# Optimization experiments

Hardware: AMD Instinct MI355X
Metric: run time of the kernel (lower is better)

## Reference

```python
import jax, jax.numpy as jnp
import numpy as np

B, Q, K, D, H = 2, 2048, 2048, 1024, 16
HD = D // H  # 64
EPS = 1e-6  # flax LayerNorm default epsilon


def setup_inputs() -> dict:
    key = jax.random.key(0)
    ks = jax.random.split(key, 12)
    s = 1.0 / np.sqrt(D)  # lecun_normal-like scale
    inputs_q = jax.random.normal(ks[0], (B, Q, D), jnp.float32)
    bias = jax.random.normal(ks[1], (B, 1, Q, K), jnp.float32)
    mask = jax.random.randint(ks[2], (B, 1, Q, K), 0, 2).astype(jnp.bool_)
    wq = jax.random.normal(ks[3], (D, H, HD), jnp.float32) * s
    wk = jax.random.normal(ks[4], (D, H, HD), jnp.float32) * s
    wv = jax.random.normal(ks[5], (D, H, HD), jnp.float32) * s
    bq = jnp.zeros((H, HD), jnp.float32)
    bk = jnp.zeros((H, HD), jnp.float32)
    bv = jnp.zeros((H, HD), jnp.float32)
    q_scale = jnp.ones((HD,), jnp.float32)
    k_scale = jnp.ones((HD,), jnp.float32)
    wo = jax.random.normal(ks[6], (H, HD, D), jnp.float32) * s
    bo = jnp.zeros((D,), jnp.float32)
    return dict(inputs_q=inputs_q, bias=bias, mask=mask, wq=wq, bq=bq,
                wk=wk, bk=bk, wv=wv, bv=bv, q_scale=q_scale, k_scale=k_scale,
                wo=wo, bo=bo)


def _layernorm_nobias(x, scale):
    # normalize over last axis (head_dim), no bias, like flax LayerNorm(use_bias=False)
    mean = jnp.mean(x, axis=-1, keepdims=True)
    var = jnp.mean(jnp.square(x - mean), axis=-1, keepdims=True)
    return (x - mean) * jax.lax.rsqrt(var + EPS) * scale


def reference(inputs_q, bias, mask, wq, bq, wk, bk, wv, bv, q_scale, k_scale, wo, bo):
    # QKV projections (self-attention: k and v inputs default to inputs_q)
    q = jnp.einsum('bqd,dhe->bqhe', inputs_q, wq) + bq  # [B,Q,H,HD]
    k = jnp.einsum('bkd,dhe->bkhe', inputs_q, wk) + bk  # [B,K,H,HD]
    v = jnp.einsum('bkd,dhe->bkhe', inputs_q, wv) + bv  # [B,K,H,HD]
    # optional QK layernorm (normalize_qk=True)
    q = _layernorm_nobias(q, q_scale)
    k = _layernorm_nobias(k, k_scale)
    # attention weights
    q = q / jnp.sqrt(jnp.asarray(q.shape[-1], q.dtype))
    attn = jnp.einsum('bqhe,bkhe->bhqk', q, k)  # [B,H,Q,K]
    attn = attn + bias
    big_neg = jnp.finfo(q.dtype).min
    attn = jnp.where(mask, attn, big_neg)
    attn = jax.nn.softmax(attn.astype(jnp.float32), axis=-1).astype(q.dtype)
    # weighted values + output projection
    x = jnp.einsum('bhqk,bkhe->bqhe', attn, v)  # [B,Q,H,HD]
    out = jnp.einsum('bqhe,heo->bqo', x, wo) + bo  # [B,Q,D]
    return out
```

## Files before the change

kernel.cpp:

```cpp
#include <hip/hip_runtime.h>
#include <cstdint>
#include <cstddef>

typedef __bf16 bf16_t;
typedef __bf16 bf16x8 __attribute__((ext_vector_type(8)));
typedef __bf16 bf16x4 __attribute__((ext_vector_type(4)));
typedef _Float16 f16_t;
typedef _Float16 f16x4 __attribute__((ext_vector_type(4)));
typedef float f32x4 __attribute__((ext_vector_type(4)));

constexpr int BB = 2, SS = 2048, DD = 1024, HH = 16, HDIM = 64;
constexpr int BS = BB * SS;
constexpr float LOG2E = 1.4426950408889634f;

__device__ __forceinline__ void glds16(const void* g, void* l) {
  __builtin_amdgcn_global_load_lds((const __attribute__((address_space(1))) void*)g,
                                   (__attribute__((address_space(3))) void*)l, 16, 0, 0);
}

__global__ __launch_bounds__(256) void prep_fused(
    const float* __restrict__ x, const float* __restrict__ wq, const float* __restrict__ wk,
    const float* __restrict__ wv, const float* __restrict__ wo, const float* __restrict__ bias,
    const int* __restrict__ mask, bf16_t* __restrict__ xb, bf16_t* __restrict__ wqkv_t,
    bf16_t* __restrict__ wo_t, f16_t* __restrict__ vmq) {
  __shared__ __align__(16) char smem[18432];
  float (*tile)[65] = (float(*)[65])smem;
  f16_t (*btile)[72] = (f16_t(*)[72])smem;
  int bid = blockIdx.x;
  int t = threadIdx.x;
  if (bid < 4096) {
    int i = bid * 256 + t;
    float4 v = ((const float4*)x)[i];
    union { bf16_t h[4]; uint2 u; } o;
    o.h[0] = (bf16_t)v.x; o.h[1] = (bf16_t)v.y; o.h[2] = (bf16_t)v.z; o.h[3] = (bf16_t)v.w;
    ((uint2*)xb)[i] = o.u;
  } else if (bid < 5120) {
    int id = bid - 4096;
    int which = id >> 8, tr = (id >> 4) & 15, tc = id & 15;
    const float* src = (which == 0) ? wq : (which == 1) ? wk : (which == 2) ? wv : wo;
    bf16_t* dst = (which < 3) ? wqkv_t : wo_t;
    int noff = (which < 3) ? which * 1024 : 0;
#pragma unroll
    for (int p = 0; p < 4; ++p) {
      int e = (p * 256 + t) * 4;
      int r = e >> 6, c = e & 63;
      float4 v = *(const float4*)&src[(size_t)(tr * 64 + r) * 1024 + tc * 64 + c];
      tile[r][c] = v.x; tile[r][c + 1] = v.y; tile[r][c + 2] = v.z; tile[r][c + 3] = v.w;
    }
    __syncthreads();
#pragma unroll
    for (int p = 0; p < 4; ++p) {
      int e = (p * 256 + t) * 4;
      int r = e >> 6, c = e & 63;
      union { bf16_t h[4]; uint2 u; } o;
#pragma unroll
      for (int j = 0; j < 4; ++j) o.h[j] = (bf16_t)tile[c + j][r];
      *(uint2*)&dst[(size_t)(noff + tc * 64 + r) * 1024 + tr * 64 + c] = o.u;
    }
  } else {
    int id = bid - 5120;
    int b = id >> 9, qt = (id >> 5) & 15, kt = id & 31;
    size_t base_in = ((size_t)(b * 2048 + qt * 128)) * 2048 + kt * 64;
#pragma unroll
    for (int p = 0; p < 4; ++p) {
      int c = p * 256 + t;
      int qr = c >> 3, k8 = (c & 7) * 8;
      const float* bp = &bias[base_in + (size_t)qr * 2048 + k8];
      const int* mp = &mask[base_in + (size_t)qr * 2048 + k8];
      float4 b0 = *(const float4*)bp;
      float4 b1 = *(const float4*)(bp + 4);
      int4 m0 = *(const int4*)mp;
      int4 m1 = *(const int4*)(mp + 4);
      union { f16_t h[8]; uint4 u; } o;
      o.h[0] = m0.x ? (f16_t)__builtin_amdgcn_exp2f(b0.x * LOG2E - 8.0f) : (f16_t)0.0f;
      o.h[1] = m0.y ? (f16_t)__builtin_amdgcn_exp2f(b0.y * LOG2E - 8.0f) : (f16_t)0.0f;
      o.h[2] = m0.z ? (f16_t)__builtin_amdgcn_exp2f(b0.z * LOG2E - 8.0f) : (f16_t)0.0f;
      o.h[3] = m0.w ? (f16_t)__builtin_amdgcn_exp2f(b0.w * LOG2E - 8.0f) : (f16_t)0.0f;
      o.h[4] = m1.x ? (f16_t)__builtin_amdgcn_exp2f(b1.x * LOG2E - 8.0f) : (f16_t)0.0f;
      o.h[5] = m1.y ? (f16_t)__builtin_amdgcn_exp2f(b1.y * LOG2E - 8.0f) : (f16_t)0.0f;
      o.h[6] = m1.z ? (f16_t)__builtin_amdgcn_exp2f(b1.z * LOG2E - 8.0f) : (f16_t)0.0f;
      o.h[7] = m1.w ? (f16_t)__builtin_amdgcn_exp2f(b1.w * LOG2E - 8.0f) : (f16_t)0.0f;
      *(uint4*)&btile[qr][k8] = o.u;
    }
    __syncthreads();
    int w = t >> 6, lane = t & 63, lo = lane & 15, quad = lane >> 4;
    size_t obase = ((size_t)(((b * 16 + qt) * 32 + kt) * 16)) * 64;
#pragma unroll
    for (int j = 0; j < 4; ++j) {
      int row = w * 32 + (j >> 1) * 16 + lo;
      int mbl = 2 * (j & 1);
      union { f16_t h[8]; uint4 u; } o;
#pragma unroll
      for (int e = 0; e < 8; ++e)
        o.h[e] = btile[row][(mbl + (e >> 2)) * 16 + quad * 4 + (e & 3)];
      ((uint4*)vmq)[obase + (w * 4 + j) * 64 + lane] = o.u;
    }
  }
}

template <bool OUT_F32, int BNT>
__global__ __launch_bounds__(256) void gemm_bt(const bf16_t* __restrict__ A,
                                               const bf16_t* __restrict__ Bt,
                                               bf16_t* __restrict__ Cb, float* __restrict__ Cf,
                                               const float* __restrict__ bias, int M, int N,
                                               int Kd) {
  constexpr int WNW = BNT / 2;
  constexpr int NFR = WNW / 16;
  __shared__ __align__(16) bf16_t As[128][32];
  __shared__ __align__(16) bf16_t Bs[BNT][32];
  int tid = threadIdx.x;
  int lane = tid & 63, w = tid >> 6;
  int lo = lane & 15, quad = lane >> 4;
  int wm = w >> 1, wn = w & 1;
  int nbx = gridDim.x;
  int nwg = nbx * gridDim.y;
  int lid = blockIdx.y * nbx + blockIdx.x;
  int sid = (lid & 7) * (nwg >> 3) + (lid >> 3);
  int m0 = (sid / nbx) * 128, n0 = (sid % nbx) * BNT;
  int srow = lane >> 2;
  int scol = (lane & 3) * 8;
  f32x4 acc[4][NFR] = {};
  for (int kk = 0; kk < Kd; kk += 32) {
#pragma unroll
    for (int t = 0; t < 2; ++t) {
      int rb = (w * 2 + t) * 16;
      glds16(&A[(size_t)(m0 + rb + srow) * Kd + kk + scol], &As[rb][0]);
      if (rb < BNT) glds16(&Bt[(size_t)(n0 + rb + srow) * Kd + kk + scol], &Bs[rb][0]);
    }
    asm volatile("s_waitcnt vmcnt(0)" ::: "memory");
    __syncthreads();
    bf16x8 am[4], bn[NFR];
#pragma unroll
    for (int i = 0; i < 4; ++i) am[i] = *(const bf16x8*)&As[wm * 64 + i * 16 + lo][quad * 8];
#pragma unroll
    for (int i = 0; i < NFR; ++i) bn[i] = *(const bf16x8*)&Bs[wn * WNW + i * 16 + lo][quad * 8];
#pragma unroll
    for (int mi = 0; mi < 4; ++mi)
#pragma unroll
      for (int ni = 0; ni < NFR; ++ni)
        acc[mi][ni] = __builtin_amdgcn_mfma_f32_16x16x32_bf16(am[mi], bn[ni], acc[mi][ni], 0, 0, 0);
    __syncthreads();
  }
#pragma unroll
  for (int mi = 0; mi < 4; ++mi) {
#pragma unroll
    for (int ni = 0; ni < NFR; ++ni) {
#pragma unroll
      for (int r = 0; r < 4; ++r) {
        int row = m0 + wm * 64 + mi * 16 + quad * 4 + r;
        int col = n0 + wn * WNW + ni * 16 + lo;
        float v = acc[mi][ni][r];
        if (OUT_F32)
          Cf[(size_t)row * N + col] = v + bias[col];
        else
          Cb[(size_t)row * N + col] = (bf16_t)v;
      }
    }
  }
}

__global__ __launch_bounds__(256) void postqkv(const bf16_t* __restrict__ Cqkv,
                                               const float* __restrict__ bq,
                                               const float* __restrict__ bk,
                                               const float* __restrict__ bv,
                                               const float* __restrict__ q_scale,
                                               const float* __restrict__ k_scale,
                                               bf16_t* __restrict__ qb, bf16_t* __restrict__ kb,
                                               f16_t* __restrict__ vt) {
  __shared__ float tile[64][65];
  int bid = blockIdx.x;
  int t = threadIdx.x;
  if (bid < 4096) {
    int mode = bid >> 11;
    int lane = t & 63;
    const float* badd = (mode == 0) ? bq : bk;
    const float* sc = (mode == 0) ? q_scale : k_scale;
    bf16_t* dst = (mode == 0) ? qb : kb;
    int vb = (bid & 2047) * 32 + (t >> 6) * 8;
#pragma unroll
    for (int i = 0; i < 8; ++i) {
      int vec = vb + i;
      int bs = vec >> 4, h = vec & 15;
      int b = bs >> 11, s = bs & 2047;
      float x = (float)Cqkv[(size_t)bs * 3072 + mode * 1024 + h * 64 + lane] + badd[h * 64 + lane];
      float sum = x;
#pragma unroll
      for (int off = 32; off >= 1; off >>= 1) sum += __shfl_xor(sum, off, 64);
      float mean = sum * (1.0f / 64.0f);
      float d = x - mean;
      float vs = d * d;
#pragma unroll
      for (int off = 32; off >= 1; off >>= 1) vs += __shfl_xor(vs, off, 64);
      float var = vs * (1.0f / 64.0f);
      float y = d * rsqrtf(var + 1e-6f) * sc[lane];
      if (mode == 0) y *= 0.125f * LOG2E;
      int el = (mode == 0) ? lane : ((((lane >> 3) ^ (s & 7)) << 3) | (lane & 7));
      dst[(size_t)((b * 16 + h) * 2048 + s) * 64 + el] = (bf16_t)y;
    }
  } else {
    int id2 = bid - 4096;
    int st = id2 & 31, h = (id2 >> 5) & 15, b = id2 >> 9;
#pragma unroll
    for (int p = 0; p < 2; ++p) {
      int e = (p * 256 + t) * 8;
      int r = e >> 6, c = e & 63;
      bf16x8 v8 = *(const bf16x8*)&Cqkv[(size_t)(b * SS + st * 64 + r) * 3072 + 2048 + h * 64 + c];
#pragma unroll
      for (int j = 0; j < 8; ++j) tile[r][c + j] = (float)v8[j] + bv[h * 64 + c + j];
    }
    __syncthreads();
#pragma unroll
    for (int p = 0; p < 2; ++p) {
      int e = (p * 256 + t) * 8;
      int r = e >> 6, c = e & 63;
      union { f16_t h[8]; uint4 u; } o;
#pragma unroll
      for (int j = 0; j < 8; ++j) o.h[j] = (f16_t)tile[c + j][r];
      *(uint4*)&vt[(size_t)((b * HH + h) * HDIM + r) * SS + st * 64 +
                   ((((c >> 3) ^ (r & 7)) << 3))] = o.u;
    }
  }
}

#define ATTN_TILE(KT, CUR, STG, VMC)                                                          \
  {                                                                                           \
    if ((KT) == 31) { asm volatile("s_waitcnt vmcnt(0)" ::: "memory"); }                      \
    else            { asm volatile("s_waitcnt vmcnt(8)" ::: "memory"); }                      \
    __builtin_amdgcn_s_barrier();                                                             \
    if ((KT) + 2 < 32) {                                                                      \
      int k0n = ((KT) + 2) * 64;                                                              \
      _Pragma("unroll") for (int tt = 0; tt < 2; ++tt) {                                      \
        int i = w * 2 + tt;                                                                   \
        int r = i * 8 + (lane >> 3);                                                          \
        glds16(&kbase[(size_t)(k0n + r) * 64 + ((lane & 7) << 3)], (STG) + i * 1024);         \
        glds16(&vbase[(size_t)r * SS + k0n + ((lane & 7) << 3)], (STG) + 8192 + i * 1024);    \
      }                                                                                       \
    }                                                                                         \
    __builtin_amdgcn_s_setprio(1);                                                            \
    bf16x8 ka[4][2];                                                                          \
    _Pragma("unroll") for (int mb = 0; mb < 4; ++mb)                                          \
      _Pragma("unroll") for (int ec = 0; ec < 2; ++ec)                                        \
        ka[mb][ec] = *(const bf16x8*)((CUR) + (mb * 16 + lo) * 128 +                          \
                                      ((((ec << 2) | quad) ^ (lo & 7)) << 4));                \
    f16x4 pf[2][4];                                                                           \
    _Pragma("unroll") for (int qg = 0; qg < 2; ++qg)                                          \
      _Pragma("unroll") for (int mb = 0; mb < 4; ++mb) {                                      \
        f32x4 s = {};                                                                         \
        s = __builtin_amdgcn_mfma_f32_16x16x32_bf16(ka[mb][0], bqf[qg][0], s, 0, 0, 0);       \
        s = __builtin_amdgcn_mfma_f32_16x16x32_bf16(ka[mb][1], bqf[qg][1], s, 0, 0, 0);       \
        f16x4 p4;                                                                             \
        p4[0] = (f16_t)__builtin_amdgcn_exp2f(fminf(s[0], 15.0f));                            \
        p4[1] = (f16_t)__builtin_amdgcn_exp2f(fminf(s[1], 15.0f));                            \
        p4[2] = (f16_t)__builtin_amdgcn_exp2f(fminf(s[2], 15.0f));                            \
        p4[3] = (f16_t)__builtin_amdgcn_exp2f(fminf(s[3], 15.0f));                            \
        pf[qg][mb] = p4 * VMC[qg * 2 + (mb >> 1)].q[mb & 1];                                  \
      }                                                                                       \
    __builtin_amdgcn_s_setprio(0);                                                            \
    if ((KT) + 2 < 32) {           \
      _Pragma("unroll") for (int j = 0; j < 4; ++j)                                           \
        VMC[j].u = vmtile[(size_t)((KT) + 2) * 1024 + j * 64];                                \
    }                                                                                         \
    __builtin_amdgcn_s_setprio(1);                                                            \
    _Pragma("unroll") for (int mb = 0; mb < 4; ++mb) {                                        \
      _Pragma("unroll") for (int eb = 0; eb < 4; ++eb) {                                      \
        f16x4 va = *(const f16x4*)((CUR) + 8192 + (eb * 16 + lo) * 128 +                      \
                                   (((((mb << 1) | (quad >> 1)) ^ (lo & 7)) << 4) |           \
                                    ((quad & 1) << 3)));                                      \
        _Pragma("unroll") for (int qg = 0; qg < 2; ++qg)                                      \
          ot[qg][eb] =                                                                        \
              __builtin_amdgcn_mfma_f32_16x16x16f16(va, pf[qg][mb], ot[qg][eb], 0, 0, 0);     \
      }                                                                                       \
      _Pragma("unroll") for (int qg = 0; qg < 2; ++qg)                                        \
        lacc[qg] = __builtin_amdgcn_mfma_f32_16x16x16f16(ones, pf[qg][mb], lacc[qg], 0, 0, 0);\
    }                                                                                         \
    __builtin_amdgcn_s_setprio(0);                                                            \
  }

__global__ __launch_bounds__(256, 2) void attn_kernel(const bf16_t* __restrict__ qb,
                                                      const bf16_t* __restrict__ kb,
                                                      const f16_t* __restrict__ vt,
                                                      const f16_t* __restrict__ vmq,
                                                      bf16_t* __restrict__ xout) {
  __shared__ __align__(16) char lds[4][16384];
  int tid = threadIdx.x;
  int lane = tid & 63, w = tid >> 6;
  int lo = lane & 15, quad = lane >> 4;
  int qt = blockIdx.x, h = blockIdx.y, b = blockIdx.z;
  size_t headoff = (size_t)(b * HH + h) * SS * HDIM;
  int q0 = qt * 128 + w * 32;
  const bf16_t* kbase = kb + headoff;
  const f16_t* vbase = vt + headoff;
  const uint4* vmtile =
      (const uint4*)vmq + ((size_t)((b * 16 + qt) * 32) * 16 + w * 4) * 64 + lane;

  bf16x8 bqf[2][2];
#pragma unroll
  for (int qg = 0; qg < 2; ++qg)
#pragma unroll
    for (int ec = 0; ec < 2; ++ec)
      bqf[qg][ec] =
          *(const bf16x8*)&qb[headoff + (size_t)(q0 + qg * 16 + lo) * HDIM + ec * 32 + quad * 8];

  f16x4 ones;
#pragma unroll
  for (int j = 0; j < 4; ++j) ones[j] = (f16_t)1.0f;

  f32x4 ot[2][4] = {};
  f32x4 lacc[2] = {};

  union VM { uint4 u; f16x4 q[2]; };
  VM vma[4], vmb[4];

#pragma unroll
  for (int tt = 0; tt < 2; ++tt) {
    int i = w * 2 + tt;
    int r = i * 8 + (lane >> 3);
    glds16(&kbase[(size_t)r * 64 + ((lane & 7) << 3)], lds[0] + i * 1024);
    glds16(&vbase[(size_t)r * SS + ((lane & 7) << 3)], lds[0] + 8192 + i * 1024);
  }
#pragma unroll
  for (int j = 0; j < 4; ++j) vma[j].u = vmtile[j * 64];
#pragma unroll
  for (int tt = 0; tt < 2; ++tt) {
    int i = w * 2 + tt;
    int r = i * 8 + (lane >> 3);
    glds16(&kbase[(size_t)(64 + r) * 64 + ((lane & 7) << 3)], lds[1] + i * 1024);
    glds16(&vbase[(size_t)r * SS + 64 + ((lane & 7) << 3)], lds[1] + 8192 + i * 1024);
  }
#pragma unroll
  for (int j = 0; j < 4; ++j) vmb[j].u = vmtile[1024 + j * 64];

#pragma unroll 1
  for (int kt0 = 0; kt0 < 32; kt0 += 4) {
    ATTN_TILE(kt0 + 0, lds[0], lds[2], vma)
    ATTN_TILE(kt0 + 1, lds[1], lds[3], vmb)
    ATTN_TILE(kt0 + 2, lds[2], lds[0], vma)
    ATTN_TILE(kt0 + 3, lds[3], lds[1], vmb)
  }

#pragma unroll
  for (int qg = 0; qg < 2; ++qg) {
    float rl = 1.0f / lacc[qg][0];
    int q = q0 + qg * 16 + lo;
#pragma unroll
    for (int eb = 0; eb < 4; ++eb) {
      union { bf16_t h4[4]; uint2 u; } o;
#pragma unroll
      for (int r = 0; r < 4; ++r) o.h4[r] = (bf16_t)(ot[qg][eb][r] * rl);
      *(uint2*)&xout[(size_t)(b * SS + q) * DD + h * 64 + eb * 16 + quad * 4] = o.u;
    }
  }
}

extern "C" void kernel_launch(void* const* d_in, const int* in_sizes, int n_in, void* d_out,
                              int out_size, void* d_ws, size_t ws_size, hipStream_t stream) {
  const float* inputs_q = (const float*)d_in[0];
  const float* bias = (const float*)d_in[1];
  const int* mask = (const int*)d_in[2];
  const float* wq = (const float*)d_in[3];
  const float* bq = (const float*)d_in[4];
  const float* wk = (const float*)d_in[5];
  const float* bk = (const float*)d_in[6];
  const float* wv = (const float*)d_in[7];
  const float* bv = (const float*)d_in[8];
  const float* q_scale = (const float*)d_in[9];
  const float* k_scale = (const float*)d_in[10];
  const float* wo = (const float*)d_in[11];
  const float* bo = (const float*)d_in[12];
  float* out = (float*)d_out;

  char* ws = (char*)d_ws;
  bf16_t* wo_t   = (bf16_t*)(ws);
  f16_t*  vmq    = (f16_t*)(ws + ((size_t)2 << 20));
  bf16_t* cqkv   = (bf16_t*)(ws + ((size_t)19 << 20));
  bf16_t* xattn  = (bf16_t*)(ws + ((size_t)19 << 20));
  bf16_t* xb     = (bf16_t*)(ws + ((size_t)43 << 20));
  bf16_t* qb2    = (bf16_t*)(ws + ((size_t)43 << 20));
  bf16_t* wqkv_t = (bf16_t*)(ws + ((size_t)51 << 20));
  bf16_t* kb2    = (bf16_t*)(ws + ((size_t)51 << 20));
  f16_t*  vtb    = (f16_t*)(ws + ((size_t)59 << 20));

  prep_fused<<<6144, 256, 0, stream>>>(inputs_q, wq, wk, wv, wo, bias, mask, xb, wqkv_t, wo_t, vmq);
  gemm_bt<false, 128><<<dim3(24, 32), 256, 0, stream>>>(xb, wqkv_t, cqkv, nullptr, nullptr, BS,
                                                        3072, DD);
  postqkv<<<5120, 256, 0, stream>>>(cqkv, bq, bk, bv, q_scale, k_scale, qb2, kb2, vtb);
  attn_kernel<<<dim3(SS / 128, HH, BB), 256, 0, stream>>>(qb2, kb2, vtb, vmq, xattn);
  gemm_bt<true, 64><<<dim3(16, 32), 256, 0, stream>>>(xattn, wo_t, nullptr, out, bo, BS, 1024, DD);
}
```

Before: 285.8 us.

## Split attention over two key halves with a merge kernel

The attention grid is split along the key dimension into two halves, doubling the block count. Each block writes unnormalized fp16 partial outputs and row sums to workspace, and a new merge kernel adds the halves and normalizes into bf16. LDS triple-buffering replaces the four buffers with rotating pointers so three blocks can fit per CU. The cost is extra global traffic for the partials, one more launch, and fp16 range risk on unnormalized accumulators (exponents are clamped, so the max-free softmax still applies).

```diff
diff --git a/kernel.cpp b/kernel.cpp
--- a/kernel.cpp
+++ b/kernel.cpp
@@ -224,10 +224,10 @@
 
 #define ATTN_TILE(KT, CUR, STG, VMC)                                                          \
   {                                                                                           \
-    if ((KT) == 31) { asm volatile("s_waitcnt vmcnt(0)" ::: "memory"); }                      \
+    if ((KT) == 15) { asm volatile("s_waitcnt vmcnt(0)" ::: "memory"); }                      \
     else            { asm volatile("s_waitcnt vmcnt(8)" ::: "memory"); }                      \
     __builtin_amdgcn_s_barrier();                                                             \
-    if ((KT) + 2 < 32) {                                                                      \
+    if ((KT) + 2 < 16) {                                                                      \
       int k0n = ((KT) + 2) * 64;                                                              \
       _Pragma("unroll") for (int tt = 0; tt < 2; ++tt) {                                      \
         int i = w * 2 + tt;                                                                   \
@@ -256,7 +256,7 @@
         pf[qg][mb] = p4 * VMC[qg * 2 + (mb >> 1)].q[mb & 1];                                  \
       }                                                                                       \
     __builtin_amdgcn_s_setprio(0);                                                            \
-    if ((KT) + 2 < 32) {           \
+    if ((KT) + 2 < 16) {           \
       _Pragma("unroll") for (int j = 0; j < 4; ++j)                                           \
         VMC[j].u = vmtile[(size_t)((KT) + 2) * 1024 + j * 64];                                \
     }                                                                                         \
@@ -276,22 +276,24 @@
     __builtin_amdgcn_s_setprio(0);                                                            \
   }
 
-__global__ __launch_bounds__(256, 2) void attn_kernel(const bf16_t* __restrict__ qb,
+__global__ __launch_bounds__(256, 3) void attn_kernel(const bf16_t* __restrict__ qb,
                                                       const bf16_t* __restrict__ kb,
                                                       const f16_t* __restrict__ vt,
                                                       const f16_t* __restrict__ vmq,
-                                                      bf16_t* __restrict__ xout) {
-  __shared__ __align__(16) char lds[4][16384];
+                                                      f16_t* __restrict__ op,
+                                                      float* __restrict__ lp) {
+  __shared__ __align__(16) char lds[3][16384];
   int tid = threadIdx.x;
   int lane = tid & 63, w = tid >> 6;
   int lo = lane & 15, quad = lane >> 4;
-  int qt = blockIdx.x, h = blockIdx.y, b = blockIdx.z;
+  int qt = blockIdx.x, h = blockIdx.y;
+  int b = blockIdx.z >> 1, kh = blockIdx.z & 1;
   size_t headoff = (size_t)(b * HH + h) * SS * HDIM;
   int q0 = qt * 128 + w * 32;
-  const bf16_t* kbase = kb + headoff;
-  const f16_t* vbase = vt + headoff;
+  const bf16_t* kbase = kb + headoff + (size_t)kh * 1024 * HDIM;
+  const f16_t* vbase = vt + headoff + (size_t)kh * 1024;
   const uint4* vmtile =
-      (const uint4*)vmq + ((size_t)((b * 16 + qt) * 32) * 16 + w * 4) * 64 + lane;
+      (const uint4*)vmq + ((size_t)((b * 16 + qt) * 32 + kh * 16) * 16 + w * 4) * 64 + lane;
 
   bf16x8 bqf[2][2];
 #pragma unroll
@@ -311,12 +313,16 @@
   union VM { uint4 u; f16x4 q[2]; };
   VM vma[4], vmb[4];
 
+  char* p0 = lds[0];
+  char* p1 = lds[1];
+  char* p2 = lds[2];
+
 #pragma unroll
   for (int tt = 0; tt < 2; ++tt) {
     int i = w * 2 + tt;
     int r = i * 8 + (lane >> 3);
-    glds16(&kbase[(size_t)r * 64 + ((lane & 7) << 3)], lds[0] + i * 1024);
-    glds16(&vbase[(size_t)r * SS + ((lane & 7) << 3)], lds[0] + 8192 + i * 1024);
+    glds16(&kbase[(size_t)r * 64 + ((lane & 7) << 3)], p0 + i * 1024);
+    glds16(&vbase[(size_t)r * SS + ((lane & 7) << 3)], p0 + 8192 + i * 1024);
   }
 #pragma unroll
   for (int j = 0; j < 4; ++j) vma[j].u = vmtile[j * 64];
@@ -324,32 +330,56 @@
   for (int tt = 0; tt < 2; ++tt) {
     int i = w * 2 + tt;
     int r = i * 8 + (lane >> 3);
-    glds16(&kbase[(size_t)(64 + r) * 64 + ((lane & 7) << 3)], lds[1] + i * 1024);
-    glds16(&vbase[(size_t)r * SS + 64 + ((lane & 7) << 3)], lds[1] + 8192 + i * 1024);
+    glds16(&kbase[(size_t)(64 + r) * 64 + ((lane & 7) << 3)], p1 + i * 1024);
+    glds16(&vbase[(size_t)r * SS + 64 + ((lane & 7) << 3)], p1 + 8192 + i * 1024);
   }
 #pragma unroll
   for (int j = 0; j < 4; ++j) vmb[j].u = vmtile[1024 + j * 64];
 
 #pragma unroll 1
-  for (int kt0 = 0; kt0 < 32; kt0 += 4) {
-    ATTN_TILE(kt0 + 0, lds[0], lds[2], vma)
-    ATTN_TILE(kt0 + 1, lds[1], lds[3], vmb)
-    ATTN_TILE(kt0 + 2, lds[2], lds[0], vma)
-    ATTN_TILE(kt0 + 3, lds[3], lds[1], vmb)
-  }
-
+  for (int kt0 = 0; kt0 < 16; kt0 += 2) {
+    ATTN_TILE(kt0 + 0, p0, p2, vma)
+    ATTN_TILE(kt0 + 1, p1, p0, vmb)
+    char* tswp = p0; p0 = p2; p2 = p1; p1 = tswp;
+  }
+
+  int bl = ((b * 2 + kh) * HH + h) * 16 + qt;
+  f16_t* opb = op + (size_t)bl * (128 * 64);
 #pragma unroll
   for (int qg = 0; qg < 2; ++qg) {
-    float rl = 1.0f / lacc[qg][0];
-    int q = q0 + qg * 16 + lo;
+    int ql = w * 32 + qg * 16 + lo;
 #pragma unroll
     for (int eb = 0; eb < 4; ++eb) {
-      union { bf16_t h4[4]; uint2 u; } o;
-#pragma unroll
-      for (int r = 0; r < 4; ++r) o.h4[r] = (bf16_t)(ot[qg][eb][r] * rl);
-      *(uint2*)&xout[(size_t)(b * SS + q) * DD + h * 64 + eb * 16 + quad * 4] = o.u;
-    }
-  }
+      union { f16_t h4[4]; uint2 u; } o;
+#pragma unroll
+      for (int r = 0; r < 4; ++r) o.h4[r] = (f16_t)ot[qg][eb][r];
+      *(uint2*)&opb[(size_t)ql * 64 + eb * 16 + quad * 4] = o.u;
+    }
+    if (quad == 0) lp[bl * 128 + ql] = lacc[qg][0];
+  }
+}
+
+__global__ __launch_bounds__(256) void merge_kernel(const f16_t* __restrict__ op,
+                                                    const float* __restrict__ lp,
+                                                    bf16_t* __restrict__ xattn) {
+  int i = blockIdx.x * 256 + threadIdx.x;
+  int bs = i >> 7;
+  int d0 = (i & 127) * 8;
+  int b = bs >> 11, q = bs & 2047;
+  int h = d0 >> 6;
+  int e0 = d0 & 63;
+  int qt = q >> 7, qloc = q & 127;
+  int bl0 = ((b * 2) * HH + h) * 16 + qt;
+  int bl1 = bl0 + 256;
+  size_t off = (size_t)qloc * 64 + e0;
+  union { f16_t h[8]; uint4 u; } a, c;
+  a.u = *(const uint4*)&op[(size_t)bl0 * (128 * 64) + off];
+  c.u = *(const uint4*)&op[(size_t)bl1 * (128 * 64) + off];
+  float rl = 1.0f / (lp[bl0 * 128 + qloc] + lp[bl1 * 128 + qloc]);
+  union { bf16_t h[8]; uint4 u; } o;
+#pragma unroll
+  for (int j = 0; j < 8; ++j) o.h[j] = (bf16_t)(((float)a.h[j] + (float)c.h[j]) * rl);
+  *(uint4*)&xattn[(size_t)bs * DD + d0] = o.u;
 }
 
 extern "C" void kernel_launch(void* const* d_in, const int* in_sizes, int n_in, void* d_out,
@@ -372,8 +402,10 @@
   char* ws = (char*)d_ws;
   bf16_t* wo_t   = (bf16_t*)(ws);
   f16_t*  vmq    = (f16_t*)(ws + ((size_t)2 << 20));
+  float*  lp     = (float*)(ws + ((size_t)18 << 20));
   bf16_t* cqkv   = (bf16_t*)(ws + ((size_t)19 << 20));
-  bf16_t* xattn  = (bf16_t*)(ws + ((size_t)19 << 20));
+  f16_t*  op     = (f16_t*)(ws + ((size_t)19 << 20));
+  bf16_t* xattn  = (bf16_t*)(ws + ((size_t)35 << 20));
   bf16_t* xb     = (bf16_t*)(ws + ((size_t)43 << 20));
   bf16_t* qb2    = (bf16_t*)(ws + ((size_t)43 << 20));
   bf16_t* wqkv_t = (bf16_t*)(ws + ((size_t)51 << 20));
@@ -384,6 +416,7 @@
   gemm_bt<false, 128><<<dim3(24, 32), 256, 0, stream>>>(xb, wqkv_t, cqkv, nullptr, nullptr, BS,
                                                         3072, DD);
   postqkv<<<5120, 256, 0, stream>>>(cqkv, bq, bk, bv, q_scale, k_scale, qb2, kb2, vtb);
-  attn_kernel<<<dim3(SS / 128, HH, BB), 256, 0, stream>>>(qb2, kb2, vtb, vmq, xattn);
+  attn_kernel<<<dim3(SS / 128, HH, BB * 2), 256, 0, stream>>>(qb2, kb2, vtb, vmq, op, lp);
+  merge_kernel<<<2048, 256, 0, stream>>>(op, lp, xattn);
   gemm_bt<true, 64><<<dim3(16, 32), 256, 0, stream>>>(xattn, wo_t, nullptr, out, bo, BS, 1024, DD);
 }
```

After: 315.1 us. +10.3%, slower.

## Load K tiles directly into registers and remap attention block order

Applied to the files above, without the earlier changes.

The attention kernel now reads K fragments straight from global memory into registers, one tile ahead, instead of staging them through LDS. Only V is still staged, using a triple-buffered 8 KB ring, and the K swizzle in postqkv is removed to match. The grid becomes 1D with a block-index remap so that consecutive blocks spread across heads and batches, which is meant to improve cache locality and XCD distribution. This cuts LDS footprint and LDS read traffic, at the cost of more vector registers, uncoalesced direct global loads of K, and hand-tuned vmcnt wait counts that must match the new load ordering.

```diff
diff --git a/kernel.cpp b/kernel.cpp
--- a/kernel.cpp
+++ b/kernel.cpp
@@ -17,6 +17,8 @@
   __builtin_amdgcn_global_load_lds((const __attribute__((address_space(1))) void*)g,
                                    (__attribute__((address_space(3))) void*)l, 16, 0, 0);
 }
+
+#define MEMFENCE asm volatile("" ::: "memory")
 
 __global__ __launch_bounds__(256) void prep_fused(
     const float* __restrict__ x, const float* __restrict__ wq, const float* __restrict__ wk,
@@ -194,8 +196,7 @@
       float var = vs * (1.0f / 64.0f);
       float y = d * rsqrtf(var + 1e-6f) * sc[lane];
       if (mode == 0) y *= 0.125f * LOG2E;
-      int el = (mode == 0) ? lane : ((((lane >> 3) ^ (s & 7)) << 3) | (lane & 7));
-      dst[(size_t)((b * 16 + h) * 2048 + s) * 64 + el] = (bf16_t)y;
+      dst[(size_t)((b * 16 + h) * 2048 + s) * 64 + lane] = (bf16_t)y;
     }
   } else {
     int id2 = bid - 4096;
@@ -222,32 +223,18 @@
   }
 }
 
-#define ATTN_TILE(KT, CUR, STG, VMC)                                                          \
+#define ATTN_TILE(KT, CURV, STGV, KC, KN, VMC)                                                \
   {                                                                                           \
-    if ((KT) == 31) { asm volatile("s_waitcnt vmcnt(0)" ::: "memory"); }                      \
-    else            { asm volatile("s_waitcnt vmcnt(8)" ::: "memory"); }                      \
+    if ((KT) == 31) { asm volatile("s_waitcnt vmcnt(8)" ::: "memory"); }                      \
+    else            { asm volatile("s_waitcnt vmcnt(14)" ::: "memory"); }                     \
     __builtin_amdgcn_s_barrier();                                                             \
-    if ((KT) + 2 < 32) {                                                                      \
-      int k0n = ((KT) + 2) * 64;                                                              \
-      _Pragma("unroll") for (int tt = 0; tt < 2; ++tt) {                                      \
-        int i = w * 2 + tt;                                                                   \
-        int r = i * 8 + (lane >> 3);                                                          \
-        glds16(&kbase[(size_t)(k0n + r) * 64 + ((lane & 7) << 3)], (STG) + i * 1024);         \
-        glds16(&vbase[(size_t)r * SS + k0n + ((lane & 7) << 3)], (STG) + 8192 + i * 1024);    \
-      }                                                                                       \
-    }                                                                                         \
     __builtin_amdgcn_s_setprio(1);                                                            \
-    bf16x8 ka[4][2];                                                                          \
-    _Pragma("unroll") for (int mb = 0; mb < 4; ++mb)                                          \
-      _Pragma("unroll") for (int ec = 0; ec < 2; ++ec)                                        \
-        ka[mb][ec] = *(const bf16x8*)((CUR) + (mb * 16 + lo) * 128 +                          \
-                                      ((((ec << 2) | quad) ^ (lo & 7)) << 4));                \
     f16x4 pf[2][4];                                                                           \
     _Pragma("unroll") for (int qg = 0; qg < 2; ++qg)                                          \
       _Pragma("unroll") for (int mb = 0; mb < 4; ++mb) {                                      \
         f32x4 s = {};                                                                         \
-        s = __builtin_amdgcn_mfma_f32_16x16x32_bf16(ka[mb][0], bqf[qg][0], s, 0, 0, 0);       \
-        s = __builtin_amdgcn_mfma_f32_16x16x32_bf16(ka[mb][1], bqf[qg][1], s, 0, 0, 0);       \
+        s = __builtin_amdgcn_mfma_f32_16x16x32_bf16(KC[mb * 2 + 0], bqf[qg][0], s, 0, 0, 0);  \
+        s = __builtin_amdgcn_mfma_f32_16x16x32_bf16(KC[mb * 2 + 1], bqf[qg][1], s, 0, 0, 0);  \
         f16x4 p4;                                                                             \
         p4[0] = (f16_t)__builtin_amdgcn_exp2f(fminf(s[0], 15.0f));                            \
         p4[1] = (f16_t)__builtin_amdgcn_exp2f(fminf(s[1], 15.0f));                            \
@@ -256,14 +243,26 @@
         pf[qg][mb] = p4 * VMC[qg * 2 + (mb >> 1)].q[mb & 1];                                  \
       }                                                                                       \
     __builtin_amdgcn_s_setprio(0);                                                            \
-    if ((KT) + 2 < 32) {           \
+    if ((KT) + 1 < 32) {        \
+      _Pragma("unroll") for (int mb = 0; mb < 4; ++mb)                                        \
+        _Pragma("unroll") for (int ec = 0; ec < 2; ++ec)                                      \
+          KN[mb * 2 + ec] = *(const bf16x8*)&kbase[(size_t)(((KT) + 1) * 64 + mb * 16 + lo) * \
+                                                       64 + ec * 32 + quad * 8];              \
+    }                                                                                         \
+    if ((KT) + 2 < 32) {                                                                      \
+      int k0n = ((KT) + 2) * 64;                                                              \
+      _Pragma("unroll") for (int tt = 0; tt < 2; ++tt) {                                      \
+        int i = w * 2 + tt;                                                                   \
+        int r = i * 8 + (lane >> 3);                                                          \
+        glds16(&vbase[(size_t)r * SS + k0n + ((lane & 7) << 3)], (STGV) + i * 1024);          \
+      }                                                                                       \
       _Pragma("unroll") for (int j = 0; j < 4; ++j)                                           \
         VMC[j].u = vmtile[(size_t)((KT) + 2) * 1024 + j * 64];                                \
     }                                                                                         \
     __builtin_amdgcn_s_setprio(1);                                                            \
     _Pragma("unroll") for (int mb = 0; mb < 4; ++mb) {                                        \
       _Pragma("unroll") for (int eb = 0; eb < 4; ++eb) {                                      \
-        f16x4 va = *(const f16x4*)((CUR) + 8192 + (eb * 16 + lo) * 128 +                      \
+        f16x4 va = *(const f16x4*)((CURV) + (eb * 16 + lo) * 128 +                            \
                                    (((((mb << 1) | (quad >> 1)) ^ (lo & 7)) << 4) |           \
                                     ((quad & 1) << 3)));                                      \
         _Pragma("unroll") for (int qg = 0; qg < 2; ++qg)                                      \
@@ -281,11 +280,13 @@
                                                       const f16_t* __restrict__ vt,
                                                       const f16_t* __restrict__ vmq,
                                                       bf16_t* __restrict__ xout) {
-  __shared__ __align__(16) char lds[4][16384];
+  __shared__ __align__(16) char ldsV[3][8192];
   int tid = threadIdx.x;
   int lane = tid & 63, w = tid >> 6;
   int lo = lane & 15, quad = lane >> 4;
-  int qt = blockIdx.x, h = blockIdx.y, b = blockIdx.z;
+  int lid = blockIdx.x;
+  int sid = ((lid & 7) << 6) | (lid >> 3);
+  int qt = sid & 15, h = (sid >> 4) & 15, b = sid >> 8;
   size_t headoff = (size_t)(b * HH + h) * SS * HDIM;
   int q0 = qt * 128 + w * 32;
   const bf16_t* kbase = kb + headoff;
@@ -310,32 +311,44 @@
 
   union VM { uint4 u; f16x4 q[2]; };
   VM vma[4], vmb[4];
+  bf16x8 kaA[8], kaB[8];
+
+  char* p0 = ldsV[0];
+  char* p1 = ldsV[1];
+  char* p2 = ldsV[2];
 
 #pragma unroll
   for (int tt = 0; tt < 2; ++tt) {
     int i = w * 2 + tt;
     int r = i * 8 + (lane >> 3);
-    glds16(&kbase[(size_t)r * 64 + ((lane & 7) << 3)], lds[0] + i * 1024);
-    glds16(&vbase[(size_t)r * SS + ((lane & 7) << 3)], lds[0] + 8192 + i * 1024);
-  }
+    glds16(&vbase[(size_t)r * SS + ((lane & 7) << 3)], p0 + i * 1024);
+  }
+  MEMFENCE;
 #pragma unroll
   for (int j = 0; j < 4; ++j) vma[j].u = vmtile[j * 64];
+  MEMFENCE;
+#pragma unroll
+  for (int mb = 0; mb < 4; ++mb)
+#pragma unroll
+    for (int ec = 0; ec < 2; ++ec)
+      kaA[mb * 2 + ec] =
+          *(const bf16x8*)&kbase[(size_t)(mb * 16 + lo) * 64 + ec * 32 + quad * 8];
+  MEMFENCE;
 #pragma unroll
   for (int tt = 0; tt < 2; ++tt) {
     int i = w * 2 + tt;
     int r = i * 8 + (lane >> 3);
-    glds16(&kbase[(size_t)(64 + r) * 64 + ((lane & 7) << 3)], lds[1] + i * 1024);
-    glds16(&vbase[(size_t)r * SS + 64 + ((lane & 7) << 3)], lds[1] + 8192 + i * 1024);
-  }
+    glds16(&vbase[(size_t)r * SS + 64 + ((lane & 7) << 3)], p1 + i * 1024);
+  }
+  MEMFENCE;
 #pragma unroll
   for (int j = 0; j < 4; ++j) vmb[j].u = vmtile[1024 + j * 64];
 
 #pragma unroll 1
-  for (int kt0 = 0; kt0 < 32; kt0 += 4) {
-    ATTN_TILE(kt0 + 0, lds[0], lds[2], vma)
-    ATTN_TILE(kt0 + 1, lds[1], lds[3], vmb)
-    ATTN_TILE(kt0 + 2, lds[2], lds[0], vma)
-    ATTN_TILE(kt0 + 3, lds[3], lds[1], vmb)
+  for (int kt0 = 0; kt0 < 32; kt0 += 2) {
+    ATTN_TILE(kt0 + 0, p0, p2, kaA, kaB, vma)
+    ATTN_TILE(kt0 + 1, p1, p0, kaB, kaA, vmb)
+    char* tswp = p0; p0 = p2; p2 = p1; p1 = tswp;
   }
 
 #pragma unroll
@@ -384,6 +397,6 @@
   gemm_bt<false, 128><<<dim3(24, 32), 256, 0, stream>>>(xb, wqkv_t, cqkv, nullptr, nullptr, BS,
                                                         3072, DD);
   postqkv<<<5120, 256, 0, stream>>>(cqkv, bq, bk, bv, q_scale, k_scale, qb2, kb2, vtb);
-  attn_kernel<<<dim3(SS / 128, HH, BB), 256, 0, stream>>>(qb2, kb2, vtb, vmq, xattn);
+  attn_kernel<<<512, 256, 0, stream>>>(qb2, kb2, vtb, vmq, xattn);
   gemm_bt<true, 64><<<dim3(16, 32), 256, 0, stream>>>(xattn, wo_t, nullptr, out, bo, BS, 1024, DD);
 }
```

New measurement: 302.3 us. +5.8%, slower.
